# Optimization experiments

Measured on AMD Instinct MI355X. Metric: run time of the kernel, lower is better.

## Reference

```python
import jax, jax.numpy as jnp
import numpy as np

B, N, C, H, W = 4, 3, 128, 128, 128
NH, NP, NL, WS, CT = 4, 4, 3, 8, 64
HD = C // NH
GROUPS = 8
DT_GAIN, MOS, EPS = 1.0, 1.5, 1e-5


def conv1x1(x, w, b):
    return jnp.einsum('bchw,oc->bohw', x, w) + b[None, :, None, None]


def group_norm(x, gamma, beta):
    b, c, h, w = x.shape
    xg = x.reshape(b, GROUPS, -1)
    mu = xg.mean(-1, keepdims=True)
    var = xg.var(-1, keepdims=True)
    xn = ((xg - mu) * jax.lax.rsqrt(var + EPS)).reshape(b, c, h, w)
    return xn * gamma[None, :, None, None] + beta[None, :, None, None]


def window_partition(x):
    b, c, h, w = x.shape
    hw, ww = h // WS, w // WS
    x = x.reshape(b, c, hw, WS, ww, WS).transpose(0, 2, 4, 1, 3, 5)
    return x.reshape(b * hw * ww, c, WS, WS)


def window_reverse(win, hw, ww, b):
    c = win.shape[1]
    x = win.reshape(b, hw, ww, c, WS, WS).transpose(0, 3, 1, 4, 2, 5)
    return x.reshape(b, c, hw * WS, ww * WS)


def bilinear_sample(v_flat, xy):
    # v_flat: [N,BW,NH,WS*WS,HD]; xy in [-1,1]: [BW,WS,WS,NH,NL,NP,2]
    # torch grid_sample, align_corners=False, padding_mode='border'
    ix = jnp.clip(((xy[..., 0] + 1.0) * WS - 1.0) * 0.5, 0.0, WS - 1.0)
    iy = jnp.clip(((xy[..., 1] + 1.0) * WS - 1.0) * 0.5, 0.0, WS - 1.0)
    x0 = jnp.floor(ix)
    y0 = jnp.floor(iy)
    wx = ix - x0
    wy = iy - y0
    x0i = x0.astype(jnp.int32)
    y0i = y0.astype(jnp.int32)
    x1i = jnp.minimum(x0i + 1, WS - 1)
    y1i = jnp.minimum(y0i + 1, WS - 1)

    def to_nbh(a):  # [BW,WS,WS,NH,NL,NP] -> [NL,BW,NH,WS*WS*NP]
        return jnp.transpose(a, (4, 0, 3, 1, 2, 5)).reshape(a.shape[4], a.shape[0], a.shape[3], -1)

    def gather(yi, xi):
        idx = to_nbh(yi * WS + xi)
        return jnp.take_along_axis(v_flat, idx[..., None], axis=3)

    wxt = to_nbh(wx)[..., None]
    wyt = to_nbh(wy)[..., None]
    top = gather(y0i, x0i) * (1.0 - wxt) + gather(y0i, x1i) * wxt
    bot = gather(y1i, x0i) * (1.0 - wxt) + gather(y1i, x1i) * wxt
    return top * (1.0 - wyt) + bot * wyt  # [NL,BW,NH,WS*WS*NP,HD]


def _forward(query, values, rel_scalar, tgt_enc, so1_w, so1_b, gno_g, gno_b,
             so2_w, so2_b, aw1_w, aw1_b, gna_g, gna_b, aw2_w, aw2_b,
             vproj_w, vproj_b, oproj_w, oproj_b, filmo_w, filmo_b,
             filma_w, filma_b, dts_w, dts_b, level_embed,
             conf1_w, conf1_b, conf2_w, conf2_b):
    Bq, Cq, Hq, Wq = query.shape
    hw, ww = Hq // WS, Wq // WS
    num_win = hw * ww
    BW = Bq * num_win
    q_win = window_partition(query)                        # [BW,C,ws,ws]
    v_all = jax.vmap(window_partition, in_axes=1)(values)  # [N,BW,C,ws,ws]

    film_o = jnp.tile(tgt_enc @ filmo_w.T + filmo_b, (num_win, 1))[:, :, None, None]
    film_a = jnp.tile(tgt_enc @ filma_w.T + filma_b, (num_win, 1))[:, :, None, None]

    offsets = conv1x1(jax.nn.relu(group_norm(conv1x1(q_win + film_o, so1_w, so1_b), gno_g, gno_b)), so2_w, so2_b)
    attn_raw = conv1x1(jax.nn.relu(group_norm(conv1x1(q_win + film_a, aw1_w, aw1_b), gna_g, gna_b)), aw2_w, aw2_b)

    attn6 = attn_raw.reshape(BW, NH, NL, NP, WS, WS).transpose(0, 4, 5, 1, 2, 3)  # [BW,ws,ws,NH,NL,NP]
    dt = rel_scalar[:, :N]
    dt_bw = jnp.tile(dt, (num_win, 1))
    bias6 = -DT_GAIN * jnp.abs(dt_bw)[:, None, None, None, :, None]
    attn = jax.nn.softmax((attn6 + bias6).reshape(BW, WS, WS, NH, NL * NP), axis=-1)
    attn6s = attn.reshape(BW, WS, WS, NH, NL, NP)

    probs = attn + 1e-8
    ent = -(probs * jnp.log(probs)).sum(-1).mean(-1)  # [BW,ws,ws]

    lin = jnp.linspace(0.0, 1.0, WS)
    yg, xg = jnp.meshgrid(lin, lin, indexing='ij')
    ref = jnp.stack([xg, yg], -1)  # [ws,ws,2]
    off = offsets.reshape(BW, NH, NL, NP, 2, WS, WS).transpose(0, 5, 6, 1, 2, 3, 4)
    xy = jnp.clip(ref[None, :, :, None, None, None, :] + off, 0.0, 1.0) * 2.0 - 1.0

    hscale = 1.0 + (MOS - 1.0) * jax.nn.sigmoid(jnp.abs(dt)[..., None] * dts_w[:, 0] + dts_b)  # [B,N,NH]
    hscale_bw = jnp.repeat(hscale, num_win, axis=0)
    xy = jnp.clip(xy * jnp.transpose(hscale_bw, (0, 2, 1))[:, None, None, :, :, None, None], -1.0, 1.0)

    v_proj = (jnp.einsum('nbchw,oc->nbohw', v_all + level_embed[:, None, :, None, None], vproj_w)
              + vproj_b[None, None, :, None, None])
    v_flat = v_proj.reshape(N, BW, NH, HD, WS * WS).transpose(0, 1, 2, 4, 3)  # [N,BW,NH,ws*ws,HD]

    sampled = bilinear_sample(v_flat, xy).reshape(N, BW, NH, WS, WS, NP, HD)
    out = jnp.einsum('nbhijpd,bijhnp->bhdij', sampled, attn6s).reshape(BW, C, WS, WS)

    fused = window_reverse(conv1x1(out, oproj_w, oproj_b), hw, ww, Bq)
    c1 = jax.lax.conv_general_dilated(fused, conf1_w, (1, 1), ((1, 1), (1, 1)),
                                      dimension_numbers=('NCHW', 'OIHW', 'NCHW')) + conf1_b[None, :, None, None]
    conf = jax.nn.sigmoid(conv1x1(jax.nn.relu(c1), conf2_w, conf2_b))
    entropy = window_reverse(ent[:, None], hw, ww, Bq)
    return fused, conf, entropy


def setup_inputs() -> dict:
    ks = jax.random.split(jax.random.key(0), 32)

    def nrm(i, shape, s=0.05):
        return jax.random.normal(ks[i], shape, jnp.float32) * s

    return dict(
        query=jax.random.normal(ks[0], (B, C, H, W), jnp.float32),
        values=jax.random.normal(ks[1], (B, N, C, H, W), jnp.float32),
        rel_scalar=jax.random.normal(ks[2], (B, N), jnp.float32),
        tgt_enc=jax.random.normal(ks[3], (B, CT), jnp.float32),
        so1_w=nrm(4, (C // 2, C)), so1_b=nrm(5, (C // 2,)),
        gno_g=jnp.ones((C // 2,), jnp.float32), gno_b=jnp.zeros((C // 2,), jnp.float32),
        so2_w=nrm(6, (NH * NL * NP * 2, C // 2)), so2_b=nrm(7, (NH * NL * NP * 2,)),
        aw1_w=nrm(8, (C // 2, C)), aw1_b=nrm(9, (C // 2,)),
        gna_g=jnp.ones((C // 2,), jnp.float32), gna_b=jnp.zeros((C // 2,), jnp.float32),
        aw2_w=nrm(10, (NH * NL * NP, C // 2)), aw2_b=nrm(11, (NH * NL * NP,)),
        vproj_w=nrm(12, (C, C)), vproj_b=nrm(13, (C,)),
        oproj_w=nrm(14, (C, C)), oproj_b=nrm(15, (C,)),
        filmo_w=nrm(16, (C, CT)), filmo_b=nrm(17, (C,)),
        filma_w=nrm(18, (C, CT)), filma_b=nrm(19, (C,)),
        dts_w=nrm(20, (NH, 1)), dts_b=nrm(21, (NH,)),
        level_embed=nrm(22, (NL, C), 0.02),
        conf1_w=nrm(23, (C // 4, C, 3, 3)), conf1_b=nrm(24, (C // 4,)),
        conf2_w=nrm(25, (1, C // 4)), conf2_b=nrm(26, (1,)),
    )


def reference(query, values, rel_scalar, tgt_enc, so1_w, so1_b, gno_g, gno_b,
              so2_w, so2_b, aw1_w, aw1_b, gna_g, gna_b, aw2_w, aw2_b,
              vproj_w, vproj_b, oproj_w, oproj_b, filmo_w, filmo_b,
              filma_w, filma_b, dts_w, dts_b, level_embed,
              conf1_w, conf1_b, conf2_w, conf2_b):
    return _forward(query, values, rel_scalar, tgt_enc, so1_w, so1_b, gno_g, gno_b,
                    so2_w, so2_b, aw1_w, aw1_b, gna_g, gna_b, aw2_w, aw2_b,
                    vproj_w, vproj_b, oproj_w, oproj_b, filmo_w, filmo_b,
                    filma_w, filma_b, dts_w, dts_b, level_embed,
                    conf1_w, conf1_b, conf2_w, conf2_b)
```

## Files before the change

### kernel.cpp

```cpp
#include <hip/hip_runtime.h>
#include <math.h>

#define NB 4
#define NVAL 3
#define NC 128
#define NHW 128
#define NHEAD 4
#define NPOINT 4
#define NLVL 3
#define WSZ 8
#define HD 32
#define NWIN 256
#define BWTOT 1024
#define NPIX 64

#define WS_SO1BA 0
#define WS_AW1BA 256
#define WS_VB    512
#define WS_HS    896
#define WS_ABSDT 944
#define WT_VP    1024
#define WT_OP    17408
#define WT_SO1   33792
#define WT_AW1   41984
#define WT_SO2   50176
#define WT_AW2   56320
#define WT_C1    59392
#define WS_COORD 96256
#define WS_ATTN  (96256 + 6291456)
#define WS_VFLAT (96256 + 6291456 + 3145728)

#define OUT_FUSED 0
#define OUT_CONF  8388608
#define OUT_ENT   (8388608 + 65536)

__device__ __forceinline__ int ufl(int x) { return __builtin_amdgcn_readfirstlane(x); }

__global__ __launch_bounds__(256) void prep_kernel(
    const float* __restrict__ tgt_enc, const float* __restrict__ filmo_w, const float* __restrict__ filmo_b,
    const float* __restrict__ filma_w, const float* __restrict__ filma_b,
    const float* __restrict__ so1_w, const float* __restrict__ so1_b,
    const float* __restrict__ aw1_w, const float* __restrict__ aw1_b,
    const float* __restrict__ so2_w, const float* __restrict__ aw2_w,
    const float* __restrict__ vproj_w, const float* __restrict__ vproj_b,
    const float* __restrict__ oproj_w, const float* __restrict__ conf1_w,
    const float* __restrict__ level_embed,
    const float* __restrict__ rel_scalar, const float* __restrict__ dts_w, const float* __restrict__ dts_b,
    float* __restrict__ ws)
{
    int tid = threadIdx.x;
    if (blockIdx.x == 0) {
        __shared__ float film[1024];
        for (int t = tid; t < 1024; t += 256) {
            int which = t >> 9; int b = (t >> 7) & 3; int c = t & 127;
            const float* fw = which ? filma_w : filmo_w;
            const float* fb = which ? filma_b : filmo_b;
            float acc = fb[c];
            for (int k = 0; k < 64; ++k) acc += tgt_enc[b * 64 + k] * fw[c * 64 + k];
            film[t] = acc;
        }
        __syncthreads();
        for (int t = tid; t < 512; t += 256) {
            int which = t >> 8; int fb = (t >> 6) & 3; int o = t & 63;
            const float* w  = which ? aw1_w : so1_w;
            const float* bb = which ? aw1_b : so1_b;
            const float* fm = &film[which * 512 + fb * 128];
            float acc = bb[o];
            for (int c = 0; c < 128; ++c) acc += w[o * 128 + c] * fm[c];
            ws[(which ? WS_AW1BA : WS_SO1BA) + fb * 64 + o] = acc;
        }
        for (int t = tid; t < 384; t += 256) {
            int n = t >> 7; int o = t & 127;
            float acc = vproj_b[o];
            for (int c = 0; c < 128; ++c) acc += level_embed[n * 128 + c] * vproj_w[o * 128 + c];
            ws[WS_VB + t] = acc;
        }
        if (tid < 48) {
            int b = tid / 12; int n = (tid / 4) % 3; int hh = tid & 3;
            float ad = fabsf(rel_scalar[b * 3 + n]);
            float s = 1.0f / (1.0f + expf(-(ad * dts_w[hh] + dts_b[hh])));
            ws[WS_HS + tid] = 1.0f + 0.5f * s;
        }
        if (tid < 12) ws[WS_ABSDT + tid] = fabsf(rel_scalar[tid]);
    } else {
        int base = (blockIdx.x - 1) * 256 + tid;
        {
            int c = base >> 7, o = base & 127;
            ws[WT_VP + base] = vproj_w[o * 128 + c];
            ws[WT_OP + base] = oproj_w[o * 128 + c];
        }
        if (base < 8192) {
            int c = base >> 6, o = base & 63;
            ws[WT_SO1 + base] = so1_w[o * 128 + c];
            ws[WT_AW1 + base] = aw1_w[o * 128 + c];
        }
        if (base < 6144) {
            int c = base / 96, o = base - c * 96;
            ws[WT_SO2 + base] = so2_w[o * 64 + c];
        }
        if (base < 3072) {
            int c = base / 48, o = base - c * 48;
            ws[WT_AW2 + base] = aw2_w[o * 64 + c];
        }
        for (int t = base; t < 36864; t += 16384) {
            int c = t / 288; int rem = t - c * 288; int k = rem / 9, tap = rem - k * 9;
            ws[WT_C1 + t] = conf1_w[(k * 128 + c) * 9 + tap];
        }
    }
}

__global__ __launch_bounds__(256) void win_kernel(
    const float* __restrict__ query,
    const float* __restrict__ so2_b,
    const float* __restrict__ gno_g, const float* __restrict__ gno_b,
    const float* __restrict__ aw2_b,
    const float* __restrict__ gna_g, const float* __restrict__ gna_b,
    float* __restrict__ ws, float* __restrict__ out)
{
    __shared__ float sA[8192];
    __shared__ float sYso[4096];
    __shared__ float sYaw[4096];

    int tid = threadIdx.x;
    int bw  = blockIdx.x;
    int b   = bw >> 8;
    int win = bw & 255;
    int wy = win >> 4, wx = win & 15;
    int fb = bw & 3;
    int pix = tid & 63;
    int og  = ufl(tid >> 6);

    const float* qbase = query + ((size_t)b << 21);
    for (int idx = tid; idx < 2048; idx += 256) {
        int c = idx >> 4, j = idx & 15;
        int row = j >> 1, half = j & 1;
        int gh = wy * 8 + row, gw0 = wx * 8 + half * 4;
        const float4 v = *(const float4*)(qbase + (c << 14) + (gh << 7) + gw0);
        *(float4*)(&sA[(c << 6) + (row << 3) + half * 4]) = v;
    }
    __syncthreads();

    {
        float accs[16], acca[16];
#pragma unroll
        for (int k = 0; k < 16; ++k) { accs[k] = 0.f; acca[k] = 0.f; }
#pragma unroll 4
        for (int c = 0; c < 128; ++c) {
            float q = sA[(c << 6) + pix];
            const float* ws1 = ws + WT_SO1 + c * 64 + og * 16;
            const float* wa1 = ws + WT_AW1 + c * 64 + og * 16;
#pragma unroll
            for (int k = 0; k < 16; ++k) {
                accs[k] += ws1[k] * q;
                acca[k] += wa1[k] * q;
            }
        }
        const float* ba_s = ws + WS_SO1BA + fb * 64;
        const float* ba_a = ws + WS_AW1BA + fb * 64;
#pragma unroll
        for (int k = 0; k < 16; ++k) {
            int o = og * 16 + k;
            sYso[(o << 6) + pix] = accs[k] + ba_s[o];
            sYaw[(o << 6) + pix] = acca[k] + ba_a[o];
        }
    }
    __syncthreads();

    {
        float s = 0.f, sq = 0.f;
        int base = tid * 16;
#pragma unroll
        for (int k = 0; k < 16; ++k) { float v = sYso[base + k]; s += v; sq += v * v; }
        sA[tid] = s; sA[256 + tid] = sq;
    }
    __syncthreads();
    if (tid < 8) {
        float s = 0.f, sq = 0.f;
        for (int k = 0; k < 32; ++k) { s += sA[tid * 32 + k]; sq += sA[256 + tid * 32 + k]; }
        float mu = s * (1.f / 512.f);
        float var = sq * (1.f / 512.f) - mu * mu;
        sA[512 + tid] = mu;
        sA[520 + tid] = 1.f / sqrtf(var + 1e-5f);
    }
    __syncthreads();
    {
        int base = tid * 16;
        int g = tid >> 5;
        int c = tid >> 2;
        float mu = sA[512 + g], rs = sA[520 + g];
        float ga = gno_g[c], be = gno_b[c];
#pragma unroll
        for (int k = 0; k < 16; ++k) {
            float v = (sYso[base + k] - mu) * rs * ga + be;
            sYso[base + k] = fmaxf(v, 0.f);
        }
    }
    __syncthreads();

    {
        float acc[24];
#pragma unroll
        for (int k = 0; k < 24; ++k) acc[k] = 0.f;
#pragma unroll 4
        for (int c = 0; c < 64; ++c) {
            float y = sYso[(c << 6) + pix];
            const float* w = ws + WT_SO2 + c * 96 + og * 24;
#pragma unroll
            for (int k = 0; k < 24; ++k) acc[k] += w[k] * y;
        }
#pragma unroll
        for (int k = 0; k < 24; ++k) {
            int ch = og * 24 + k;
            sA[1024 + (ch << 6) + pix] = acc[k] + so2_b[ch];
        }
    }
    __syncthreads();

    {
        int hh = og;
        int btrue = bw >> 8;
        float refx = (float)(pix & 7) * (1.f / 7.f);
        float refy = (float)(pix >> 3) * (1.f / 7.f);
        float* co = ws + WS_COORD + ((((size_t)bw * 64 + pix) * 4 + hh) * 24);
#pragma unroll
        for (int l = 0; l < 3; ++l) {
            float hs = ws[WS_HS + (btrue * 3 + l) * 4 + hh];
#pragma unroll
            for (int p = 0; p < 4; ++p) {
                int chx = ((hh * 3 + l) * 4 + p) * 2;
                float ox = sA[1024 + (chx << 6) + pix];
                float oy = sA[1024 + ((chx + 1) << 6) + pix];
                float x = fminf(fmaxf(refx + ox, 0.f), 1.f) * 2.f - 1.f;
                float y = fminf(fmaxf(refy + oy, 0.f), 1.f) * 2.f - 1.f;
                x = fminf(fmaxf(x * hs, -1.f), 1.f);
                y = fminf(fmaxf(y * hs, -1.f), 1.f);
                float ix = fminf(fmaxf(((x + 1.f) * 8.f - 1.f) * 0.5f, 0.f), 7.f);
                float iy = fminf(fmaxf(((y + 1.f) * 8.f - 1.f) * 0.5f, 0.f), 7.f);
                co[(l * 4 + p) * 2]     = ix;
                co[(l * 4 + p) * 2 + 1] = iy;
            }
        }
    }
    {
        float s = 0.f, sq = 0.f;
        int base = tid * 16;
#pragma unroll
        for (int k = 0; k < 16; ++k) { float v = sYaw[base + k]; s += v; sq += v * v; }
        sA[tid] = s; sA[256 + tid] = sq;
    }
    __syncthreads();
    if (tid < 8) {
        float s = 0.f, sq = 0.f;
        for (int k = 0; k < 32; ++k) { s += sA[tid * 32 + k]; sq += sA[256 + tid * 32 + k]; }
        float mu = s * (1.f / 512.f);
        float var = sq * (1.f / 512.f) - mu * mu;
        sA[512 + tid] = mu;
        sA[520 + tid] = 1.f / sqrtf(var + 1e-5f);
    }
    __syncthreads();
    {
        int base = tid * 16;
        int g = tid >> 5;
        int c = tid >> 2;
        float mu = sA[512 + g], rs = sA[520 + g];
        float ga = gna_g[c], be = gna_b[c];
#pragma unroll
        for (int k = 0; k < 16; ++k) {
            float v = (sYaw[base + k] - mu) * rs * ga + be;
            sYaw[base + k] = fmaxf(v, 0.f);
        }
    }
    __syncthreads();

    {
        float acc[12];
#pragma unroll
        for (int k = 0; k < 12; ++k) acc[k] = 0.f;
#pragma unroll 4
        for (int c = 0; c < 64; ++c) {
            float y = sYaw[(c << 6) + pix];
            const float* w = ws + WT_AW2 + c * 48 + og * 12;
#pragma unroll
            for (int k = 0; k < 12; ++k) acc[k] += w[k] * y;
        }
        __syncthreads();
#pragma unroll
        for (int k = 0; k < 12; ++k) {
            int ch = og * 12 + k;
            sA[1024 + (ch << 6) + pix] = acc[k] + aw2_b[ch];
        }
    }
    __syncthreads();

    {
        int hh = og;
        const float* ad = ws + WS_ABSDT + fb * 3;
        float lg[12];
        float m = -1e30f;
#pragma unroll
        for (int q = 0; q < 12; ++q) {
            float v = sA[1024 + (((hh * 12 + q)) << 6) + pix] - ad[q >> 2];
            lg[q] = v; m = fmaxf(m, v);
        }
        float sum = 0.f;
#pragma unroll
        for (int q = 0; q < 12; ++q) { lg[q] = expf(lg[q] - m); sum += lg[q]; }
        float inv = 1.f / sum;
        float* at = ws + WS_ATTN + ((((size_t)bw * 64 + pix) * 4 + hh) * 12);
        float hent = 0.f;
#pragma unroll
        for (int q = 0; q < 12; ++q) {
            float p = lg[q] * inv;
            at[q] = p;
            float pp = p + 1e-8f;
            hent -= pp * logf(pp);
        }
        sA[pix * 4 + hh] = hent;
    }
    __syncthreads();
    if (tid < 64) {
        float e = 0.25f * (sA[tid * 4] + sA[tid * 4 + 1] + sA[tid * 4 + 2] + sA[tid * 4 + 3]);
        int gh = wy * 8 + (tid >> 3), gw = wx * 8 + (tid & 7);
        out[OUT_ENT + (b << 14) + (gh << 7) + gw] = e;
    }
}

__global__ __launch_bounds__(256) void vproj_kernel(
    const float* __restrict__ values, float* __restrict__ ws)
{
    __shared__ float sbuf[8448];
    int tid = threadIdx.x;
    int bid = blockIdx.x;
    int n = bid >> 10;
    int bw = bid & 1023;
    int b = bw >> 8; int win = bw & 255;
    int wy = win >> 4, wx = win & 15;
    const float* vbase = values + ((size_t)(b * 3 + n) << 21);
    for (int idx = tid; idx < 2048; idx += 256) {
        int c = idx >> 4, j = idx & 15;
        int row = j >> 1, half = j & 1;
        int gh = wy * 8 + row, gw0 = wx * 8 + half * 4;
        const float4 v = *(const float4*)(vbase + (c << 14) + (gh << 7) + gw0);
        *(float4*)(&sbuf[(c << 6) + (row << 3) + half * 4]) = v;
    }
    int pix = tid & 63;
    int og = ufl(tid >> 6);
    float vbr[32];
    {
        const float* vb = ws + WS_VB + n * 128 + og * 32;
#pragma unroll
        for (int k = 0; k < 32; ++k) vbr[k] = vb[k];
    }
    __syncthreads();
    float acc[32];
#pragma unroll
    for (int k = 0; k < 32; ++k) acc[k] = 0.f;
#pragma unroll 4
    for (int c = 0; c < 128; ++c) {
        float v = sbuf[(c << 6) + pix];
        const float* w = ws + WT_VP + c * 128 + og * 32;
#pragma unroll
        for (int k = 0; k < 32; ++k) acc[k] += w[k] * v;
    }
    __syncthreads();
    int row = (og << 6) + pix;
#pragma unroll
    for (int k = 0; k < 32; ++k) sbuf[row * 33 + k] = acc[k] + vbr[k];
    __syncthreads();
    float* base2 = ws + WS_VFLAT + ((((size_t)n << 10) + bw) << 13);
#pragma unroll
    for (int i = 0; i < 8; ++i) {
        int f4 = (i * 256 + tid) * 4;
        int r = f4 >> 5, k = f4 & 31;
        float4 v = make_float4(sbuf[r * 33 + k], sbuf[r * 33 + k + 1],
                               sbuf[r * 33 + k + 2], sbuf[r * 33 + k + 3]);
        *(float4*)(base2 + f4) = v;
    }
}

__global__ __launch_bounds__(256) void sample_kernel(
    const float* __restrict__ oproj_b,
    float* __restrict__ ws, float* __restrict__ out)
{
    __shared__ float smem[17408];
    int tid = threadIdx.x;
    int bw = blockIdx.x;
    int b = bw >> 8; int win = bw & 255;
    int wy = win >> 4, wx = win & 15;
    int d  = tid & 31;
    int hh = (tid >> 5) & 3;
    int ph = tid >> 7;

    {
        const float* co = ws + WS_COORD + (size_t)bw * 6144;
        const float* at = ws + WS_ATTN + (size_t)bw * 3072;
        for (int i = tid; i < 1536; i += 256)
            *(float4*)(&smem[i * 4]) = *(const float4*)(co + i * 4);
        for (int i = tid; i < 768; i += 256)
            *(float4*)(&smem[6144 + i * 4]) = *(const float4*)(at + i * 4);
    }

    float acc[32];
#pragma unroll
    for (int q = 0; q < 32; ++q) acc[q] = 0.f;

    for (int l = 0; l < 3; ++l) {
        if (l) __syncthreads();
        const float* vsrc = ws + WS_VFLAT + ((((size_t)l << 10) + bw) << 13);
        for (int i = tid; i < 2048; i += 256)
            *(float4*)(&smem[9216 + i * 4]) = *(const float4*)(vsrc + i * 4);
        __syncthreads();

        const float* vb = &smem[9216 + hh * 2048 + d];
        for (int q = 0; q < 32; ++q) {
            int pix = ph * 32 + q;
            const float* c24 = &smem[(pix * 4 + hh) * 24 + l * 8];
            const float* a4  = &smem[6144 + (pix * 4 + hh) * 12 + l * 4];
            float a0 = 0.f;
#pragma unroll
            for (int p = 0; p < 4; ++p) {
                float ix = c24[p * 2];
                float iy = c24[p * 2 + 1];
                float a  = a4[p];
                float x0f = floorf(ix), y0f = floorf(iy);
                int x0 = (int)x0f, y0 = (int)y0f;
                float wxf = ix - x0f, wyf = iy - y0f;
                int x1 = x0 + 1; if (x1 > 7) x1 = 7;
                int y1 = y0 + 1; if (y1 > 7) y1 = 7;
                float v00 = vb[(((y0 << 3) + x0) << 5)];
                float v01 = vb[(((y0 << 3) + x1) << 5)];
                float v10 = vb[(((y1 << 3) + x0) << 5)];
                float v11 = vb[(((y1 << 3) + x1) << 5)];
                float top = v00 + (v01 - v00) * wxf;
                float bot = v10 + (v11 - v10) * wxf;
                a0 += a * (top + (bot - top) * wyf);
            }
            acc[q] += a0;
        }
    }
    __syncthreads();

#pragma unroll
    for (int q = 0; q < 32; ++q)
        smem[(hh * 32 + d) * 65 + ph * 32 + q] = acc[q];
    __syncthreads();

    int pix = tid & 63;
    int og = ufl(tid >> 6);
    float acc2[32];
#pragma unroll
    for (int k = 0; k < 32; ++k) acc2[k] = 0.f;
#pragma unroll 4
    for (int c = 0; c < 128; ++c) {
        float v = smem[c * 65 + pix];
        const float* w = ws + WT_OP + c * 128 + og * 32;
#pragma unroll
        for (int k = 0; k < 32; ++k) acc2[k] += w[k] * v;
    }
    int gh = wy * 8 + (pix >> 3), gw = wx * 8 + (pix & 7);
#pragma unroll
    for (int k = 0; k < 32; ++k) {
        int o = og * 32 + k;
        out[OUT_FUSED + ((size_t)(b * 128 + o) << 14) + (gh << 7) + gw] = acc2[k] + oproj_b[o];
    }
}

__global__ __launch_bounds__(256) void conf_kernel(
    const float* __restrict__ fused, const float* __restrict__ conf1_b,
    const float* __restrict__ conf2_w, const float* __restrict__ conf2_b,
    const float* __restrict__ ws, float* __restrict__ out)
{
    __shared__ float tile[64 * 110];
    __shared__ float red[4][64];
    int tid = threadIdx.x;
    int bid = blockIdx.x;
    int b = bid >> 8;
    int t = bid & 255; int ty = t >> 4, tx = t & 15;
    int pix = tid & 63;
    int kg  = ufl(tid >> 6);
    int py = pix >> 3, px = pix & 7;
    int oy = ty * 8, ox = tx * 8;
    const float* fin = fused + ((size_t)b << 21);

    float acc[8];
#pragma unroll
    for (int j = 0; j < 8; ++j) acc[j] = 0.f;

    for (int cc = 0; cc < 2; ++cc) {
        __syncthreads();
        for (int idx = tid; idx < 6400; idx += 256) {
            int c = idx / 100;
            int rem = idx - c * 100;
            int r = rem / 10, col = rem - r * 10;
            int gy = oy + r - 1, gx = ox + col - 1;
            float v = 0.f;
            if (gy >= 0 && gy < 128 && gx >= 0 && gx < 128)
                v = fin[((size_t)(cc * 64 + c) << 14) + (gy << 7) + gx];
            tile[c * 110 + r * 11 + col] = v;
        }
        __syncthreads();
        for (int c = 0; c < 64; ++c) {
            float v[9];
#pragma unroll
            for (int dy = 0; dy < 3; ++dy)
#pragma unroll
                for (int dx = 0; dx < 3; ++dx)
                    v[dy * 3 + dx] = tile[c * 110 + (py + dy) * 11 + (px + dx)];
            const float* wp = ws + WT_C1 + ufl((cc * 64 + c) * 288 + kg * 72);
#pragma unroll
            for (int j = 0; j < 8; ++j) {
#pragma unroll
                for (int tap = 0; tap < 9; ++tap)
                    acc[j] += v[tap] * wp[j * 9 + tap];
            }
        }
    }
    float s = 0.f;
#pragma unroll
    for (int j = 0; j < 8; ++j) {
        int k = kg * 8 + j;
        s += fmaxf(acc[j] + conf1_b[k], 0.f) * conf2_w[k];
    }
    red[kg][pix] = s;
    __syncthreads();
    if (tid < 64) {
        float tot = red[0][tid] + red[1][tid] + red[2][tid] + red[3][tid] + conf2_b[0];
        float cf = 1.f / (1.f + expf(-tot));
        int gy = oy + (tid >> 3), gx = ox + (tid & 7);
        out[OUT_CONF + (b << 14) + (gy << 7) + gx] = cf;
    }
}

extern "C" void kernel_launch(void* const* d_in, const int* in_sizes, int n_in,
                              void* d_out, int out_size, void* d_ws, size_t ws_size,
                              hipStream_t stream) {
    const float* query      = (const float*)d_in[0];
    const float* values     = (const float*)d_in[1];
    const float* rel_scalar = (const float*)d_in[2];
    const float* tgt_enc    = (const float*)d_in[3];
    const float* so1_w = (const float*)d_in[4];
    const float* so1_b = (const float*)d_in[5];
    const float* gno_g = (const float*)d_in[6];
    const float* gno_b = (const float*)d_in[7];
    const float* so2_w = (const float*)d_in[8];
    const float* so2_b = (const float*)d_in[9];
    const float* aw1_w = (const float*)d_in[10];
    const float* aw1_b = (const float*)d_in[11];
    const float* gna_g = (const float*)d_in[12];
    const float* gna_b = (const float*)d_in[13];
    const float* aw2_w = (const float*)d_in[14];
    const float* aw2_b = (const float*)d_in[15];
    const float* vproj_w = (const float*)d_in[16];
    const float* vproj_b = (const float*)d_in[17];
    const float* oproj_w = (const float*)d_in[18];
    const float* oproj_b = (const float*)d_in[19];
    const float* filmo_w = (const float*)d_in[20];
    const float* filmo_b = (const float*)d_in[21];
    const float* filma_w = (const float*)d_in[22];
    const float* filma_b = (const float*)d_in[23];
    const float* dts_w   = (const float*)d_in[24];
    const float* dts_b   = (const float*)d_in[25];
    const float* level_embed = (const float*)d_in[26];
    const float* conf1_w = (const float*)d_in[27];
    const float* conf1_b = (const float*)d_in[28];
    const float* conf2_w = (const float*)d_in[29];
    const float* conf2_b = (const float*)d_in[30];

    float* ws  = (float*)d_ws;
    float* out = (float*)d_out;

    prep_kernel<<<65, 256, 0, stream>>>(tgt_enc, filmo_w, filmo_b, filma_w, filma_b,
                                        so1_w, so1_b, aw1_w, aw1_b,
                                        so2_w, aw2_w,
                                        vproj_w, vproj_b, oproj_w, conf1_w,
                                        level_embed, rel_scalar, dts_w, dts_b, ws);
    win_kernel<<<BWTOT, 256, 0, stream>>>(query, so2_b, gno_g, gno_b,
                                          aw2_b, gna_g, gna_b, ws, out);
    vproj_kernel<<<NVAL * BWTOT, 256, 0, stream>>>(values, ws);
    sample_kernel<<<BWTOT, 256, 0, stream>>>(oproj_b, ws, out);
    conf_kernel<<<NB * 256, 256, 0, stream>>>(out, conf1_b, conf2_w, conf2_b, ws, out);
}
```

Before: 700.5 us.

## Remap sample kernel threads to pixel-head with vectorized float4 channel gathers

The bilinear sampling kernel now assigns each thread one (pixel, head) pair and accumulates all 32 head channels in registers, reading padded value rows as float4 from LDS. Coordinates and attention weights are read straight from global memory instead of being staged in shared memory, which cuts the LDS footprint. The bilinear weights are precomputed per point. A launch-bounds occupancy hint of 4 blocks is also added. In exchange, the gather addresses now differ per lane, which may cause LDS bank conflicts, and register pressure rises.

```diff
diff --git a/kernel.cpp b/kernel.cpp
--- a/kernel.cpp
+++ b/kernel.cpp
@@ -378,89 +378,91 @@
     }
 }
 
-__global__ __launch_bounds__(256) void sample_kernel(
+__global__ __launch_bounds__(256, 4) void sample_kernel(
     const float* __restrict__ oproj_b,
     float* __restrict__ ws, float* __restrict__ out)
 {
-    __shared__ float smem[17408];
+    __shared__ float smem[9216];
     int tid = threadIdx.x;
     int bw = blockIdx.x;
     int b = bw >> 8; int win = bw & 255;
     int wy = win >> 4, wx = win & 15;
-    int d  = tid & 31;
-    int hh = (tid >> 5) & 3;
-    int ph = tid >> 7;
-
-    {
-        const float* co = ws + WS_COORD + (size_t)bw * 6144;
-        const float* at = ws + WS_ATTN + (size_t)bw * 3072;
-        for (int i = tid; i < 1536; i += 256)
-            *(float4*)(&smem[i * 4]) = *(const float4*)(co + i * 4);
-        for (int i = tid; i < 768; i += 256)
-            *(float4*)(&smem[6144 + i * 4]) = *(const float4*)(at + i * 4);
-    }
+    int pix = tid & 63;
+    int hh = ufl(tid >> 6);
+
+    const float* co = ws + WS_COORD + ((size_t)(bw * 64 + pix) * 4 + hh) * 24;
+    const float* at = ws + WS_ATTN  + ((size_t)(bw * 64 + pix) * 4 + hh) * 12;
 
     float acc[32];
 #pragma unroll
-    for (int q = 0; q < 32; ++q) acc[q] = 0.f;
+    for (int k = 0; k < 32; ++k) acc[k] = 0.f;
 
     for (int l = 0; l < 3; ++l) {
+        float4 cxy0 = *(const float4*)(co + l * 8);
+        float4 cxy1 = *(const float4*)(co + l * 8 + 4);
+        float4 a4   = *(const float4*)(at + l * 4);
         if (l) __syncthreads();
         const float* vsrc = ws + WS_VFLAT + ((((size_t)l << 10) + bw) << 13);
-        for (int i = tid; i < 2048; i += 256)
-            *(float4*)(&smem[9216 + i * 4]) = *(const float4*)(vsrc + i * 4);
+        for (int i = tid; i < 2048; i += 256) {
+            float4 v = *(const float4*)(vsrc + i * 4);
+            int r = i >> 3, c4 = (i & 7) << 2;
+            *(float4*)(&smem[r * 36 + c4]) = v;
+        }
         __syncthreads();
 
-        const float* vb = &smem[9216 + hh * 2048 + d];
-        for (int q = 0; q < 32; ++q) {
-            int pix = ph * 32 + q;
-            const float* c24 = &smem[(pix * 4 + hh) * 24 + l * 8];
-            const float* a4  = &smem[6144 + (pix * 4 + hh) * 12 + l * 4];
-            float a0 = 0.f;
-#pragma unroll
-            for (int p = 0; p < 4; ++p) {
-                float ix = c24[p * 2];
-                float iy = c24[p * 2 + 1];
-                float a  = a4[p];
-                float x0f = floorf(ix), y0f = floorf(iy);
-                int x0 = (int)x0f, y0 = (int)y0f;
-                float wxf = ix - x0f, wyf = iy - y0f;
-                int x1 = x0 + 1; if (x1 > 7) x1 = 7;
-                int y1 = y0 + 1; if (y1 > 7) y1 = 7;
-                float v00 = vb[(((y0 << 3) + x0) << 5)];
-                float v01 = vb[(((y0 << 3) + x1) << 5)];
-                float v10 = vb[(((y1 << 3) + x0) << 5)];
-                float v11 = vb[(((y1 << 3) + x1) << 5)];
-                float top = v00 + (v01 - v00) * wxf;
-                float bot = v10 + (v11 - v10) * wxf;
-                a0 += a * (top + (bot - top) * wyf);
+        const float* vb = &smem[hh * (64 * 36)];
+        float ixs[4] = {cxy0.x, cxy0.z, cxy1.x, cxy1.z};
+        float iys[4] = {cxy0.y, cxy0.w, cxy1.y, cxy1.w};
+        float as4[4] = {a4.x, a4.y, a4.z, a4.w};
+#pragma unroll
+        for (int p = 0; p < 4; ++p) {
+            float ix = ixs[p], iy = iys[p], a = as4[p];
+            float x0f = floorf(ix), y0f = floorf(iy);
+            int x0 = (int)x0f, y0 = (int)y0f;
+            float wxf = ix - x0f, wyf = iy - y0f;
+            int x1 = x0 + 1; if (x1 > 7) x1 = 7;
+            int y1 = y0 + 1; if (y1 > 7) y1 = 7;
+            float w00 = a * (1.f - wxf) * (1.f - wyf);
+            float w01 = a * wxf * (1.f - wyf);
+            float w10 = a * (1.f - wxf) * wyf;
+            float w11 = a * wxf * wyf;
+            const float* r00 = vb + ((y0 << 3) + x0) * 36;
+            const float* r01 = vb + ((y0 << 3) + x1) * 36;
+            const float* r10 = vb + ((y1 << 3) + x0) * 36;
+            const float* r11 = vb + ((y1 << 3) + x1) * 36;
+#pragma unroll
+            for (int ch = 0; ch < 8; ++ch) {
+                float4 v00 = *(const float4*)(r00 + (ch << 2));
+                float4 v01 = *(const float4*)(r01 + (ch << 2));
+                float4 v10 = *(const float4*)(r10 + (ch << 2));
+                float4 v11 = *(const float4*)(r11 + (ch << 2));
+                acc[(ch << 2) + 0] += w00 * v00.x + w01 * v01.x + w10 * v10.x + w11 * v11.x;
+                acc[(ch << 2) + 1] += w00 * v00.y + w01 * v01.y + w10 * v10.y + w11 * v11.y;
+                acc[(ch << 2) + 2] += w00 * v00.z + w01 * v01.z + w10 * v10.z + w11 * v11.z;
+                acc[(ch << 2) + 3] += w00 * v00.w + w01 * v01.w + w10 * v10.w + w11 * v11.w;
             }
-            acc[q] += a0;
-        }
-    }
-    __syncthreads();
-
-#pragma unroll
-    for (int q = 0; q < 32; ++q)
-        smem[(hh * 32 + d) * 65 + ph * 32 + q] = acc[q];
-    __syncthreads();
-
-    int pix = tid & 63;
-    int og = ufl(tid >> 6);
+        }
+    }
+    __syncthreads();
+#pragma unroll
+    for (int k = 0; k < 32; ++k)
+        smem[(hh * 32 + k) * 65 + pix] = acc[k];
+    __syncthreads();
+
     float acc2[32];
 #pragma unroll
     for (int k = 0; k < 32; ++k) acc2[k] = 0.f;
 #pragma unroll 4
     for (int c = 0; c < 128; ++c) {
         float v = smem[c * 65 + pix];
-        const float* w = ws + WT_OP + c * 128 + og * 32;
+        const float* w = ws + WT_OP + c * 128 + hh * 32;
 #pragma unroll
         for (int k = 0; k < 32; ++k) acc2[k] += w[k] * v;
     }
     int gh = wy * 8 + (pix >> 3), gw = wx * 8 + (pix & 7);
 #pragma unroll
     for (int k = 0; k < 32; ++k) {
-        int o = og * 32 + k;
+        int o = hh * 32 + k;
         out[OUT_FUSED + ((size_t)(b * 128 + o) << 14) + (gh << 7) + gw] = acc2[k] + oproj_b[o];
     }
 }
```

New measurement: 659.7 us. -5.8%, faster.
